# Kernel optimization log

Measured on AMD Instinct MI355X. Metric: run time of the kernel, lower is better.

Reference implementation:

```python
import jax, jax.numpy as jnp
import numpy as np

B, CIN, H, W = 32, 512, 64, 64
HID, A, C = 256, 9, 20
M = 65536


def setup_inputs() -> dict:
    key = jax.random.key(0)
    k = jax.random.split(key, 7)
    N = B * A * H * W
    features = jax.random.normal(k[0], (B, CIN, H, W), jnp.float32)
    W1 = jax.random.normal(k[1], (HID, CIN), jnp.float32) * 0.02
    b1 = jnp.zeros((HID,), jnp.float32)
    W2 = jax.random.normal(k[2], (5 * A + C, HID), jnp.float32) * 0.02
    b2 = jnp.zeros((5 * A + C,), jnp.float32)
    pos_anchor_idx = jax.random.randint(k[3], (M,), 0, N, jnp.int64 if jax.config.read('jax_enable_x64') else jnp.int32)
    neg_anchor_idx = jax.random.randint(k[4], (M,), 0, N, jnp.int64 if jax.config.read('jax_enable_x64') else jnp.int32)
    return {"features": features, "W1": W1, "b1": b1, "W2": W2, "b2": b2,
            "pos_anchor_idx": pos_anchor_idx, "neg_anchor_idx": neg_anchor_idx}


def reference(features, W1, b1, W2, b2, pos_anchor_idx, neg_anchor_idx):
    Bb, Cin, Hh, Ww = features.shape
    # 1x1 convs are channel GEMMs
    h = jnp.einsum('bchw,oc->bohw', features, W1) + b1[None, :, None, None]
    h = jax.nn.leaky_relu(h, 0.01)  # Dropout2d identity at inference
    out = jnp.einsum('bchw,oc->bohw', h, W2) + b2[None, :, None, None]
    class_scores = out[:, 5 * A:, :, :]                      # (B, C, H, W)
    anchor = out[:, :5 * A, :, :].reshape(Bb, A, 5, Hh, Ww)   # (B, A, 5, H, W)
    conf = jax.nn.sigmoid(anchor[:, :, 0:1])                  # (B, A, 1, H, W)
    off = anchor[:, :, 1:]                                    # (B, A, 4, H, W)
    off = jnp.concatenate([jax.nn.sigmoid(off[:, :, :2]) - 0.5, off[:, :, 2:]], axis=2)
    # extraction: flat layout is b*A*H*W + a*H*W + h*W + w (permute 0,1,3,4,2)
    off_flat = off.transpose(0, 1, 3, 4, 2).reshape(-1, 4)
    conf_flat = conf.transpose(0, 1, 3, 4, 2).reshape(-1, 1)
    offsets = off_flat[pos_anchor_idx]                        # (M, 4)
    conf_out = jnp.concatenate([conf_flat[pos_anchor_idx], conf_flat[neg_anchor_idx]], axis=0)  # (2M, 1)
    # class scores: expand over A is a pure broadcast, so index by (b, spatial) directly
    b_idx = pos_anchor_idx // (A * Hh * Ww)
    sp = pos_anchor_idx % (Hh * Ww)
    cls_flat = class_scores.transpose(0, 2, 3, 1).reshape(Bb * Hh * Ww, -1)
    class_out = cls_flat[b_idx * (Hh * Ww) + sp]              # (M, C)
    return conf_out, offsets, class_out
```

## Files before the change

kernel.cpp:

```cpp
#include <hip/hip_runtime.h>
#include <hip/hip_bf16.h>

typedef __attribute__((ext_vector_type(8)))  __bf16 bf16x8;
typedef __attribute__((ext_vector_type(4)))  __bf16 bf16x4;
typedef __attribute__((ext_vector_type(16))) float  f32x16;
typedef __attribute__((ext_vector_type(4)))  float  f32x4;

#define B_    32
#define CIN   512
#define HID   256
#define HW    4096
#define NA    9
#define NCH   65
#define NPADC 96
#define BN    128
#define M_    65536
#define NTOT  (B_*NA*HW)


static __device__ __forceinline__ float sigf(float v) {
    return 1.f / (1.f + __expf(-v));
}

__global__ void prep_weights(const float* __restrict__ W1, const float* __restrict__ W2,
                             unsigned short* __restrict__ W1bt, unsigned short* __restrict__ W2p) {
    int i = blockIdx.x * 256 + threadIdx.x;
    if (i < 16*256*32) {
        int kt = i >> 13, o = (i >> 5) & 255, kk = i & 31;
        __bf16 h = (__bf16)W1[o*CIN + kt*32 + kk];
        W1bt[i] = __builtin_bit_cast(unsigned short, h);
    } else {
        int j = i - 16*256*32;
        if (j < NPADC*HID) {
            int o = j >> 8, c = j & 255;
            float v = (o < NCH) ? W2[o*HID + c] : 0.f;
            __bf16 h = (__bf16)v;
            W2p[j] = __builtin_bit_cast(unsigned short, h);
        }
    }
}

__launch_bounds__(256, 2)
__global__ void fused_mlp(const float* __restrict__ feat,
                          const float* __restrict__ b1,
                          const float* __restrict__ b2,
                          const unsigned short* __restrict__ W1bt,
                          const unsigned short* __restrict__ W2p,
                          float* __restrict__ conf_d,
                          unsigned short* __restrict__ off_w,
                          unsigned short* __restrict__ cls_w) {
    __shared__ __align__(16) unsigned char smem[65536];

    const int tid  = threadIdx.x;
    const int w    = tid >> 6;
    const int lane = tid & 63;
    const int lr   = lane & 31;
    const int lh   = lane >> 5;
    const int bidx = blockIdx.x >> 5;
    const int hw0  = (blockIdx.x & 31) * BN;

    const float* fb = feat + (size_t)bidx * CIN * HW + hw0;

    const int sB  = tid & 127;
    const int kgB = tid >> 7;

    f32x16 acc[2][4];
#pragma unroll
    for (int m = 0; m < 2; ++m)
#pragma unroll
        for (int n = 0; n < 4; ++n) acc[m][n] = (f32x16)0.f;

    float  pb[2][16];
    bf16x8 aw[2][4];

    auto issueB = [&](int kt, int s) {
#pragma unroll
        for (int q = 0; q < 2; ++q) {
            const float* src = fb + (size_t)(kt*32 + (kgB + 2*q)*8) * HW + sB;
#pragma unroll
            for (int j = 0; j < 8; ++j) pb[s][q*8 + j] = src[(size_t)j * HW];
        }
    };
    auto issueA = [&](int kt, int s) {
#pragma unroll
        for (int kk = 0; kk < 2; ++kk)
#pragma unroll
            for (int m = 0; m < 2; ++m)
                aw[s][kk*2 + m] = *(const bf16x8*)(W1bt + kt*8192 + (64*w + 32*m + lr)*32 + kk*16 + lh*8);
    };
    auto storeB = [&](int s) {
        unsigned short* Bst = (unsigned short*)(smem + s*10240);
#pragma unroll
        for (int q = 0; q < 2; ++q) {
            bf16x8 v8;
#pragma unroll
            for (int j = 0; j < 8; ++j) v8[j] = (__bf16)pb[s][q*8 + j];
            *(bf16x8*)(Bst + sB*40 + (kgB + 2*q)*8) = v8;
        }
    };

    issueB(0, 0); issueB(1, 1); issueA(0, 0);
    storeB(0);
    __syncthreads();

#pragma unroll
    for (int kt = 0; kt < 16; ++kt) {
        const int cur = kt & 1, nxt = cur ^ 1;
        if (kt + 2 < 16) issueB(kt + 2, cur);
        if (kt + 1 < 16) issueA(kt + 1, nxt);
        const unsigned short* Bst = (const unsigned short*)(smem + cur*10240);
#pragma unroll
        for (int kk = 0; kk < 2; ++kk) {
            bf16x8 a0 = aw[cur][kk*2 + 0];
            bf16x8 a1 = aw[cur][kk*2 + 1];
#pragma unroll
            for (int n = 0; n < 4; ++n) {
                bf16x8 bv = *(const bf16x8*)(Bst + (32*n + lr)*40 + kk*16 + lh*8);
                acc[0][n] = __builtin_amdgcn_mfma_f32_32x32x16_bf16(a0, bv, acc[0][n], 0, 0, 0);
                acc[1][n] = __builtin_amdgcn_mfma_f32_32x32x16_bf16(a1, bv, acc[1][n], 0, 0, 0);
            }
        }
        if (kt + 1 < 16) storeB(nxt);
        __syncthreads();
    }

#pragma unroll
    for (int m = 0; m < 2; ++m)
#pragma unroll
        for (int n = 0; n < 4; ++n) {
            int col = 32*n + lr;
            unsigned cswz = (unsigned)((col & 7) << 4);
#pragma unroll
            for (int g = 0; g < 4; ++g) {
                int rbase = 64*w + 32*m + 8*g + 4*lh;
                f32x4 b1v = *(const f32x4*)(b1 + rbase);
                bf16x4 pk;
#pragma unroll
                for (int r = 0; r < 4; ++r) {
                    float v = acc[m][n][4*g + r] + b1v[r];
                    v = v > 0.f ? v : 0.01f * v;
                    pk[r] = (__bf16)v;
                }
                unsigned addr = (unsigned)(col*512 + rbase*2) ^ cswz;
                *(bf16x4*)(smem + addr) = pk;
            }
        }
    __syncthreads();

    f32x16 acc2[3];
#pragma unroll
    for (int m = 0; m < 3; ++m) acc2[m] = (f32x16)0.f;
    const int col2 = 32*w + lr;
    const unsigned cswz2 = (unsigned)((col2 & 7) << 4);
    for (int kt2 = 0; kt2 < 8; ++kt2) {
#pragma unroll
        for (int kk = 0; kk < 2; ++kk) {
            int k0 = kt2*32 + kk*16 + lh*8;
            bf16x8 bv = *(const bf16x8*)(smem + ((unsigned)(col2*512 + k0*2) ^ cswz2));
#pragma unroll
            for (int m = 0; m < 3; ++m) {
                bf16x8 av = *(const bf16x8*)(W2p + (32*m + lr)*256 + k0);
                acc2[m] = __builtin_amdgcn_mfma_f32_32x32x16_bf16(av, bv, acc2[m], 0, 0, 0);
            }
        }
    }

    __syncthreads();
    float* so = (float*)smem;
#pragma unroll
    for (int m = 0; m < 3; ++m)
#pragma unroll
        for (int g = 0; g < 4; ++g) {
            int rbase = 32*m + 8*g + 4*lh;
            if (rbase <= 64) {
#pragma unroll
                for (int r = 0; r < 4; ++r) {
                    int row = rbase + r;
                    if (row < NCH) so[row*128 + col2] = acc2[m][4*g + r] + b2[row];
                }
            }
        }
    __syncthreads();

    {
        const int p   = tid & 127;
        const int phw = hw0 + p;
        const int b9  = bidx * NA;
        if (tid < 128) {
#pragma unroll
            for (int a = 0; a < 9; ++a) {
                float v0 = so[(5*a+0)*128 + p];
                float v1 = so[(5*a+1)*128 + p];
                float v2 = so[(5*a+2)*128 + p];
                float v3 = so[(5*a+3)*128 + p];
                float v4 = so[(5*a+4)*128 + p];
                int abase = ((b9 + a) << 12) + phw;
                conf_d[abase] = sigf(v0);
                bf16x4 o;
                o[0] = (__bf16)(sigf(v1) - 0.5f);
                o[1] = (__bf16)(sigf(v2) - 0.5f);
                o[2] = (__bf16)v3;
                o[3] = (__bf16)v4;
                *(bf16x4*)(off_w + ((size_t)abase << 2)) = o;
            }
        } else {
            unsigned short* dst = cls_w + ((size_t)((bidx << 12) + phw) << 5);
#pragma unroll
            for (int q = 0; q < 4; ++q) {
                bf16x8 v;
#pragma unroll
                for (int r = 0; r < 8; ++r) {
                    int c = q*8 + r;
                    v[r] = (c < 20) ? (__bf16)so[(45 + c)*128 + p] : (__bf16)0.f;
                }
                *(bf16x8*)(dst + q*8) = v;
            }
        }
    }
}

__global__ void gather_all(const int* __restrict__ pos, const int* __restrict__ neg,
                           const float* __restrict__ conf_d,
                           const unsigned short* __restrict__ off_w,
                           const unsigned short* __restrict__ cls_w,
                           float* __restrict__ out) {
    int t = blockIdx.x * 256 + threadIdx.x;
    if (t < 2*M_) {
        int idx = (t < M_) ? pos[t] : neg[t - M_];
        out[t] = conf_d[idx];
    } else if (t < 3*M_) {
        int i = t - 2*M_;
        int p = pos[i];
        bf16x4 o = *(const bf16x4*)(off_w + ((size_t)p << 2));
        f32x4 f;
        f[0] = (float)o[0]; f[1] = (float)o[1];
        f[2] = (float)o[2]; f[3] = (float)o[3];
        *(f32x4*)(out + 2*(size_t)M_ + 4*(size_t)i) = f;
    } else {
        int i = t - 3*M_;
        int p = pos[i];
        int hw = p & 4095;
        int b  = (p >> 12) / 9;
        const unsigned short* src = cls_w + ((size_t)((b << 12) + hw) << 5);
        float* dst = out + 6*(size_t)M_ + 20*(size_t)i;
        bf16x8 v0 = *(const bf16x8*)(src);
        bf16x8 v1 = *(const bf16x8*)(src + 8);
        bf16x4 v2 = *(const bf16x4*)(src + 16);
        f32x4 f;
        f[0] = (float)v0[0]; f[1] = (float)v0[1]; f[2] = (float)v0[2]; f[3] = (float)v0[3];
        *(f32x4*)(dst) = f;
        f[0] = (float)v0[4]; f[1] = (float)v0[5]; f[2] = (float)v0[6]; f[3] = (float)v0[7];
        *(f32x4*)(dst + 4) = f;
        f[0] = (float)v1[0]; f[1] = (float)v1[1]; f[2] = (float)v1[2]; f[3] = (float)v1[3];
        *(f32x4*)(dst + 8) = f;
        f[0] = (float)v1[4]; f[1] = (float)v1[5]; f[2] = (float)v1[6]; f[3] = (float)v1[7];
        *(f32x4*)(dst + 12) = f;
        f[0] = (float)v2[0]; f[1] = (float)v2[1]; f[2] = (float)v2[2]; f[3] = (float)v2[3];
        *(f32x4*)(dst + 16) = f;
    }
}

extern "C" void kernel_launch(void* const* d_in, const int* in_sizes, int n_in,
                              void* d_out, int out_size, void* d_ws, size_t ws_size,
                              hipStream_t stream) {
    const float* feat = (const float*)d_in[0];
    const float* W1   = (const float*)d_in[1];
    const float* b1   = (const float*)d_in[2];
    const float* W2   = (const float*)d_in[3];
    const float* b2   = (const float*)d_in[4];
    const int*   pos  = (const int*)d_in[5];
    const int*   neg  = (const int*)d_in[6];
    float* out = (float*)d_out;

    char* ws = (char*)d_ws;
    unsigned short* W1bt = (unsigned short*)ws;
    unsigned short* W2p  = (unsigned short*)(ws + 262144);
    float*          conf_d = (float*)(ws + 311296);
    unsigned short* off_w  = (unsigned short*)(ws + 5029888);
    unsigned short* cls_w  = (unsigned short*)(ws + 14467072);

    prep_weights<<<608, 256, 0, stream>>>(W1, W2, W1bt, W2p);
    fused_mlp<<<1024, 256, 0, stream>>>(feat, b1, b2, W1bt, W2p, conf_d, off_w, cls_w);
    gather_all<<<1024, 256, 0, stream>>>(pos, neg, conf_d, off_w, cls_w, out);
}
```

Baseline: 99.70 us.

## Give each wave its own pixel columns and drop block-wide LDS staging and barriers

Each wave now owns 32 pixel columns and all 256 hidden rows. It loads feature data straight into registers as the MFMA B operand and reads W1 fragments directly from global memory, so the shared-memory B tile and the per-iteration __syncthreads go away. The hidden activations and the second-layer outputs are staged in a per-wave LDS slice, and waves only wait on their own LDS counters. This removes block barriers and LDS traffic, but every wave now re-reads the whole W1 tile each k-step, which raises global/L2 load volume. It also uses more accumulator registers (8 f32x16), which may hurt occupancy.

```diff
diff --git a/kernel.cpp b/kernel.cpp
--- a/kernel.cpp
+++ b/kernel.cpp
@@ -58,143 +58,113 @@
     const int lh   = lane >> 5;
     const int bidx = blockIdx.x >> 5;
     const int hw0  = (blockIdx.x & 31) * BN;
-
-    const float* fb = feat + (size_t)bidx * CIN * HW + hw0;
-
-    const int sB  = tid & 127;
-    const int kgB = tid >> 7;
-
-    f32x16 acc[2][4];
-#pragma unroll
-    for (int m = 0; m < 2; ++m)
-#pragma unroll
-        for (int n = 0; n < 4; ++n) acc[m][n] = (f32x16)0.f;
-
-    float  pb[2][16];
-    bf16x8 aw[2][4];
+    const int col  = hw0 + 32*w + lr;
+
+    const float* fb = feat + (size_t)bidx * CIN * HW + col;
+    unsigned char* myLds = smem + (w << 14);
+
+    f32x16 acc[8];
+#pragma unroll
+    for (int mb = 0; mb < 8; ++mb) acc[mb] = (f32x16)0.f;
+
+    float pb[2][16];
 
     auto issueB = [&](int kt, int s) {
 #pragma unroll
-        for (int q = 0; q < 2; ++q) {
-            const float* src = fb + (size_t)(kt*32 + (kgB + 2*q)*8) * HW + sB;
-#pragma unroll
-            for (int j = 0; j < 8; ++j) pb[s][q*8 + j] = src[(size_t)j * HW];
+        for (int kk = 0; kk < 2; ++kk) {
+            const float* src = fb + (size_t)(kt*32 + kk*16 + lh*8) * HW;
+#pragma unroll
+            for (int j = 0; j < 8; ++j) pb[s][kk*8 + j] = src[(size_t)j * HW];
         }
     };
-    auto issueA = [&](int kt, int s) {
+
+    issueB(0, 0);
+
+#pragma unroll
+    for (int kt = 0; kt < 16; ++kt) {
+        const int cur = kt & 1;
+        bf16x8 aw[16];
+#pragma unroll
+        for (int mb = 0; mb < 8; ++mb)
+#pragma unroll
+            for (int kk = 0; kk < 2; ++kk)
+                aw[mb*2 + kk] = *(const bf16x8*)(W1bt + kt*8192 + (32*mb + lr)*32 + kk*16 + lh*8);
+        if (kt < 15) issueB(kt + 1, cur ^ 1);
+        bf16x8 bv[2];
 #pragma unroll
         for (int kk = 0; kk < 2; ++kk)
 #pragma unroll
-            for (int m = 0; m < 2; ++m)
-                aw[s][kk*2 + m] = *(const bf16x8*)(W1bt + kt*8192 + (64*w + 32*m + lr)*32 + kk*16 + lh*8);
-    };
-    auto storeB = [&](int s) {
-        unsigned short* Bst = (unsigned short*)(smem + s*10240);
-#pragma unroll
-        for (int q = 0; q < 2; ++q) {
-            bf16x8 v8;
-#pragma unroll
-            for (int j = 0; j < 8; ++j) v8[j] = (__bf16)pb[s][q*8 + j];
-            *(bf16x8*)(Bst + sB*40 + (kgB + 2*q)*8) = v8;
-        }
-    };
-
-    issueB(0, 0); issueB(1, 1); issueA(0, 0);
-    storeB(0);
-    __syncthreads();
-
-#pragma unroll
-    for (int kt = 0; kt < 16; ++kt) {
-        const int cur = kt & 1, nxt = cur ^ 1;
-        if (kt + 2 < 16) issueB(kt + 2, cur);
-        if (kt + 1 < 16) issueA(kt + 1, nxt);
-        const unsigned short* Bst = (const unsigned short*)(smem + cur*10240);
-#pragma unroll
-        for (int kk = 0; kk < 2; ++kk) {
-            bf16x8 a0 = aw[cur][kk*2 + 0];
-            bf16x8 a1 = aw[cur][kk*2 + 1];
-#pragma unroll
-            for (int n = 0; n < 4; ++n) {
-                bf16x8 bv = *(const bf16x8*)(Bst + (32*n + lr)*40 + kk*16 + lh*8);
-                acc[0][n] = __builtin_amdgcn_mfma_f32_32x32x16_bf16(a0, bv, acc[0][n], 0, 0, 0);
-                acc[1][n] = __builtin_amdgcn_mfma_f32_32x32x16_bf16(a1, bv, acc[1][n], 0, 0, 0);
-            }
-        }
-        if (kt + 1 < 16) storeB(nxt);
-        __syncthreads();
-    }
-
-#pragma unroll
-    for (int m = 0; m < 2; ++m)
-#pragma unroll
-        for (int n = 0; n < 4; ++n) {
-            int col = 32*n + lr;
-            unsigned cswz = (unsigned)((col & 7) << 4);
-#pragma unroll
-            for (int g = 0; g < 4; ++g) {
-                int rbase = 64*w + 32*m + 8*g + 4*lh;
-                f32x4 b1v = *(const f32x4*)(b1 + rbase);
-                bf16x4 pk;
-#pragma unroll
-                for (int r = 0; r < 4; ++r) {
-                    float v = acc[m][n][4*g + r] + b1v[r];
-                    v = v > 0.f ? v : 0.01f * v;
-                    pk[r] = (__bf16)v;
-                }
-                unsigned addr = (unsigned)(col*512 + rbase*2) ^ cswz;
-                *(bf16x4*)(smem + addr) = pk;
-            }
-        }
-    __syncthreads();
+            for (int j = 0; j < 8; ++j) bv[kk][j] = (__bf16)pb[cur][kk*8 + j];
+#pragma unroll
+        for (int kk = 0; kk < 2; ++kk)
+#pragma unroll
+            for (int mb = 0; mb < 8; ++mb)
+                acc[mb] = __builtin_amdgcn_mfma_f32_32x32x16_bf16(aw[mb*2 + kk], bv[kk], acc[mb], 0, 0, 0);
+    }
+
+    const unsigned cswz = (unsigned)((lr & 7) << 4);
+#pragma unroll
+    for (int mb = 0; mb < 8; ++mb)
+#pragma unroll
+        for (int g = 0; g < 4; ++g) {
+            int r0 = 32*mb + 8*g + 4*lh;
+            f32x4 b1v = *(const f32x4*)(b1 + r0);
+            bf16x4 pk;
+#pragma unroll
+            for (int r = 0; r < 4; ++r) {
+                float v = acc[mb][4*g + r] + b1v[r];
+                v = v > 0.f ? v : 0.01f * v;
+                pk[r] = (__bf16)v;
+            }
+            *(bf16x4*)(myLds + ((unsigned)(lr*512 + r0*2) ^ cswz)) = pk;
+        }
+    asm volatile("s_waitcnt lgkmcnt(0)" ::: "memory");
+    __builtin_amdgcn_sched_barrier(0);
 
     f32x16 acc2[3];
 #pragma unroll
     for (int m = 0; m < 3; ++m) acc2[m] = (f32x16)0.f;
-    const int col2 = 32*w + lr;
-    const unsigned cswz2 = (unsigned)((col2 & 7) << 4);
     for (int kt2 = 0; kt2 < 8; ++kt2) {
 #pragma unroll
         for (int kk = 0; kk < 2; ++kk) {
             int k0 = kt2*32 + kk*16 + lh*8;
-            bf16x8 bv = *(const bf16x8*)(smem + ((unsigned)(col2*512 + k0*2) ^ cswz2));
+            bf16x8 bv2 = *(const bf16x8*)(myLds + ((unsigned)(lr*512 + k0*2) ^ cswz));
 #pragma unroll
             for (int m = 0; m < 3; ++m) {
                 bf16x8 av = *(const bf16x8*)(W2p + (32*m + lr)*256 + k0);
-                acc2[m] = __builtin_amdgcn_mfma_f32_32x32x16_bf16(av, bv, acc2[m], 0, 0, 0);
-            }
-        }
-    }
-
-    __syncthreads();
-    float* so = (float*)smem;
+                acc2[m] = __builtin_amdgcn_mfma_f32_32x32x16_bf16(av, bv2, acc2[m], 0, 0, 0);
+            }
+        }
+    }
+    asm volatile("s_waitcnt lgkmcnt(0)" ::: "memory");
+    __builtin_amdgcn_sched_barrier(0);
+
+    float* sow = (float*)myLds;
 #pragma unroll
     for (int m = 0; m < 3; ++m)
 #pragma unroll
         for (int g = 0; g < 4; ++g) {
-            int rbase = 32*m + 8*g + 4*lh;
-            if (rbase <= 64) {
-#pragma unroll
-                for (int r = 0; r < 4; ++r) {
-                    int row = rbase + r;
-                    if (row < NCH) so[row*128 + col2] = acc2[m][4*g + r] + b2[row];
-                }
-            }
-        }
-    __syncthreads();
+            int r0 = 32*m + 8*g + 4*lh;
+#pragma unroll
+            for (int r = 0; r < 4; ++r) {
+                int row = r0 + r;
+                if (row < NCH) sow[row*36 + lr] = acc2[m][4*g + r] + b2[row];
+            }
+        }
+    asm volatile("s_waitcnt lgkmcnt(0)" ::: "memory");
+    __builtin_amdgcn_sched_barrier(0);
 
     {
-        const int p   = tid & 127;
-        const int phw = hw0 + p;
-        const int b9  = bidx * NA;
-        if (tid < 128) {
+        const int b9 = bidx * NA;
+        if (lh == 0) {
 #pragma unroll
             for (int a = 0; a < 9; ++a) {
-                float v0 = so[(5*a+0)*128 + p];
-                float v1 = so[(5*a+1)*128 + p];
-                float v2 = so[(5*a+2)*128 + p];
-                float v3 = so[(5*a+3)*128 + p];
-                float v4 = so[(5*a+4)*128 + p];
-                int abase = ((b9 + a) << 12) + phw;
+                float v0 = sow[(5*a+0)*36 + lr];
+                float v1 = sow[(5*a+1)*36 + lr];
+                float v2 = sow[(5*a+2)*36 + lr];
+                float v3 = sow[(5*a+3)*36 + lr];
+                float v4 = sow[(5*a+4)*36 + lr];
+                int abase = ((b9 + a) << 12) + col;
                 conf_d[abase] = sigf(v0);
                 bf16x4 o;
                 o[0] = (__bf16)(sigf(v1) - 0.5f);
@@ -204,14 +174,14 @@
                 *(bf16x4*)(off_w + ((size_t)abase << 2)) = o;
             }
         } else {
-            unsigned short* dst = cls_w + ((size_t)((bidx << 12) + phw) << 5);
+            unsigned short* dst = cls_w + ((size_t)((bidx << 12) + col) << 5);
 #pragma unroll
             for (int q = 0; q < 4; ++q) {
                 bf16x8 v;
 #pragma unroll
                 for (int r = 0; r < 8; ++r) {
                     int c = q*8 + r;
-                    v[r] = (c < 20) ? (__bf16)so[(45 + c)*128 + p] : (__bf16)0.f;
+                    v[r] = (c < 20) ? (__bf16)sow[(45 + c)*36 + lr] : (__bf16)0.f;
                 }
                 *(bf16x8*)(dst + q*8) = v;
             }
```

Measured after the change: 153.5 us. 54.0% more time.
